# Kernel optimization log

Hardware: AMD Instinct MI355X
Metric: run time of the kernel (lower is better)

Reference implementation:

```python
import jax, jax.numpy as jnp
import numpy as np

B, S, D, H, DEG = 4, 2048, 1024, 4096, 4  # batch, seq, n_embd, hidden, chebyshev degree
LN_EPS = 1e-5


def cheb_basis(x, degree):
    """Chebyshev polynomials T_0..T_degree of x (values assumed in [-1,1]).
    x: [..., d] -> [..., d, degree+1] via the recurrence T_k = 2x T_{k-1} - T_{k-2}."""
    T = [jnp.ones_like(x), x]
    for _ in range(2, degree + 1):
        T.append(2.0 * x * T[-1] - T[-2])
    return jnp.stack(T[: degree + 1], axis=-1)


def kan_layer(x, coef, degree):
    # x: [N, in_dim], coef: [in_dim, out_dim, degree+1] -> [N, out_dim]
    basis = cheb_basis(x, degree)  # [N, in_dim, degree+1]
    return jnp.einsum('nik,iok->no', basis, coef)


def setup_inputs() -> dict:
    key = jax.random.key(0)
    k1, k2, k3 = jax.random.split(key, 3)
    x = jax.random.normal(k1, (B, S, D), dtype=jnp.float32)
    # Chebyshev-KAN coefficient init ~ N(0, 1/(in_dim*(degree+1)))
    coef_fc = jax.random.normal(k2, (D, H, DEG + 1), dtype=jnp.float32) / np.sqrt(D * (DEG + 1))
    coef_proj = jax.random.normal(k3, (H, D, DEG + 1), dtype=jnp.float32) / np.sqrt(H * (DEG + 1))
    gamma = jnp.ones((H,), dtype=jnp.float32)
    beta = jnp.zeros((H,), dtype=jnp.float32)
    return {"x": x, "coef_fc": coef_fc, "coef_proj": coef_proj, "gamma": gamma, "beta": beta}


def reference(x, coef_fc, coef_proj, gamma, beta):
    b, s, d = x.shape
    xf = jnp.tanh(x.reshape(-1, d))                 # squash into Chebyshev domain [-1,1]
    h = kan_layer(xf, coef_fc, DEG)                 # [N, H]
    mu = jnp.mean(h, axis=-1, keepdims=True)
    var = jnp.mean(jnp.square(h - mu), axis=-1, keepdims=True)
    h = (h - mu) * jax.lax.rsqrt(var + LN_EPS) * gamma + beta
    h = jnp.tanh(h)
    out = kan_layer(h, coef_proj, DEG)              # [N, D]
    return out.reshape(b, s, d)                     # dropout is identity at eval
```

## Files before the change

kernel.cpp:

```cpp
#include <hip/hip_runtime.h>
#include <hip/hip_bf16.h>
#include <cstdint>
#include <cstddef>

typedef __bf16 bf16;
typedef __attribute__((ext_vector_type(4))) __bf16 bf16x4;
typedef __attribute__((ext_vector_type(8))) __bf16 bf16x8;
typedef __attribute__((ext_vector_type(4))) float f32x4;

#define NR 8192
#define DIM_D 1024
#define DIM_H 4096


__device__ __forceinline__ void gload_lds16(const void* g, void* l) {
  __builtin_amdgcn_global_load_lds(
      (const __attribute__((address_space(1))) void*)g,
      (__attribute__((address_space(3))) void*)l, 16, 0, 0);
}

#define BAR()  __builtin_amdgcn_s_barrier()
#define WLG0() asm volatile("s_waitcnt lgkmcnt(0)" ::: "memory")
#define WVM0() asm volatile("s_waitcnt vmcnt(0)" ::: "memory")
#define WVM4() asm volatile("s_waitcnt vmcnt(4)" ::: "memory")
#define WVM6() asm volatile("s_waitcnt vmcnt(6)" ::: "memory")
#define WVM8() asm volatile("s_waitcnt vmcnt(8)" ::: "memory")
#define PRIO1() __builtin_amdgcn_s_setprio(1)
#define PRIO0() __builtin_amdgcn_s_setprio(0)


template <int IN, int OUT>
__global__ __launch_bounds__(256) void k_prep_t(const float* __restrict__ coef,
                                                bf16* __restrict__ Bp,
                                                float* __restrict__ bpart) {
  constexpr int KT = (IN / 32) * 2;
  const int tid   = threadIdx.x;
  const int o     = blockIdx.x * 256 + tid;
  const int nb    = blockIdx.x;
  const int chunk = blockIdx.y;
  const int i0    = chunk * 32;

  float bacc = 0.f;
#pragma unroll
  for (int q = 0; q < 4; ++q) {
    bf16x8 w1, w2, w3, w4;
#pragma unroll
    for (int j = 0; j < 8; ++j) {
      const float* s = coef + ((size_t)(i0 + q * 8 + j) * OUT + o) * 5;
      bacc += s[0];
      w1[j] = (bf16)s[1]; w2[j] = (bf16)s[2]; w3[j] = (bf16)s[3]; w4[j] = (bf16)s[4];
    }
    bf16* base = Bp + ((size_t)nb * KT + chunk * 2) * 16384 + (size_t)tid * 8;
    *(bf16x8*)(base + (0 * 4 + q) * 2048)         = w1;
    *(bf16x8*)(base + (1 * 4 + q) * 2048)         = w2;
    *(bf16x8*)(base + 16384 + (0 * 4 + q) * 2048) = w3;
    *(bf16x8*)(base + 16384 + (1 * 4 + q) * 2048) = w4;
  }
  bpart[(size_t)chunk * OUT + o] = bacc;
}

__global__ __launch_bounds__(256) void k_bias_red(const float* __restrict__ bpart,
                                                  float* __restrict__ bias,
                                                  const int OUT, const int NP) {
  const int o = blockIdx.x * 256 + threadIdx.x;
  float s = 0.f;
  for (int p = 0; p < NP; ++p) s += bpart[(size_t)p * OUT + o];
  bias[o] = s;
}

__global__ __launch_bounds__(256) void k_tanh_cheb_t(const float* __restrict__ x,
                                                     bf16* __restrict__ Ap) {
  const int mb    = blockIdx.x;
  const int chunk = blockIdx.y;
  const int r     = threadIdx.x;

  const float* src = x + (size_t)(mb * 256 + r) * DIM_D + chunk * 32;
  float a[32];
#pragma unroll
  for (int u = 0; u < 8; ++u) {
    const float4 v = *(const float4*)(src + u * 4);
    a[u * 4 + 0] = tanhf(v.x);
    a[u * 4 + 1] = tanhf(v.y);
    a[u * 4 + 2] = tanhf(v.z);
    a[u * 4 + 3] = tanhf(v.w);
  }
  bf16* base = Ap + ((size_t)mb * 64 + chunk * 2) * 16384 + (size_t)r * 8;
#pragma unroll
  for (int q = 0; q < 4; ++q) {
    bf16x8 w1, w2, w3, w4;
#pragma unroll
    for (int j = 0; j < 8; ++j) {
      const float t = a[q * 8 + j], t2 = t * t;
      w1[j] = (bf16)t;
      w2[j] = (bf16)(2.f * t2 - 1.f);
      w3[j] = (bf16)(t * (4.f * t2 - 3.f));
      w4[j] = (bf16)(8.f * t2 * (t2 - 1.f) + 1.f);
    }
    *(bf16x8*)(base + (0 * 4 + q) * 2048)         = w1;
    *(bf16x8*)(base + (1 * 4 + q) * 2048)         = w2;
    *(bf16x8*)(base + 16384 + (0 * 4 + q) * 2048) = w3;
    *(bf16x8*)(base + 16384 + (1 * 4 + q) * 2048) = w4;
  }
}

__global__ __launch_bounds__(256) void k_ln_tanh(const float* __restrict__ h,
                                                 const float* __restrict__ gamma,
                                                 const float* __restrict__ beta,
                                                 bf16* __restrict__ th) {
  const int n = blockIdx.x;
  const int t = threadIdx.x;
  const float* row = h + (size_t)n * DIM_H;

  float4 v[4];
  float s1 = 0.f, s2 = 0.f;
#pragma unroll
  for (int j = 0; j < 4; ++j) {
    v[j] = *(const float4*)(row + t * 16 + j * 4);
    s1 += v[j].x + v[j].y + v[j].z + v[j].w;
    s2 += v[j].x * v[j].x + v[j].y * v[j].y + v[j].z * v[j].z + v[j].w * v[j].w;
  }
#pragma unroll
  for (int off = 32; off >= 1; off >>= 1) {
    s1 += __shfl_xor(s1, off);
    s2 += __shfl_xor(s2, off);
  }
  __shared__ float red[8];
  if ((t & 63) == 0) { red[(t >> 6) * 2] = s1; red[(t >> 6) * 2 + 1] = s2; }
  __syncthreads();
  const float S1 = red[0] + red[2] + red[4] + red[6];
  const float S2 = red[1] + red[3] + red[5] + red[7];
  const float mu   = S1 * (1.f / DIM_H);
  const float var  = S2 * (1.f / DIM_H) - mu * mu;
  const float rstd = rsqrtf(var + 1e-5f);

  float tmp[16];
#pragma unroll
  for (int j = 0; j < 4; ++j) {
    const float4 g = *(const float4*)(gamma + t * 16 + j * 4);
    const float4 b = *(const float4*)(beta  + t * 16 + j * 4);
    tmp[j * 4 + 0] = tanhf((v[j].x - mu) * rstd * g.x + b.x);
    tmp[j * 4 + 1] = tanhf((v[j].y - mu) * rstd * g.y + b.y);
    tmp[j * 4 + 2] = tanhf((v[j].z - mu) * rstd * g.z + b.z);
    tmp[j * 4 + 3] = tanhf((v[j].w - mu) * rstd * g.w + b.w);
  }
  bf16x8 w0, w1;
#pragma unroll
  for (int j = 0; j < 8; ++j) { w0[j] = (bf16)tmp[j]; w1[j] = (bf16)tmp[8 + j]; }
  bf16* o = th + (size_t)n * DIM_H + t * 16;
  *(bf16x8*)o       = w0;
  *(bf16x8*)(o + 8) = w1;
}

template <int IND, int NZ, int GX, typename CT>
__global__ __launch_bounds__(512, 2) void k_gemm8x(const bf16* __restrict__ Ap,
                                                   const bf16* __restrict__ Bp,
                                                   CT* __restrict__ C,
                                                   const float* __restrict__ bias,
                                                   const int NN) {
  constexpr int NCH = IND / 32 / NZ;
  constexpr int KTt = (IND / 32) * 2;
  constexpr int TOT = GX * 32 * NZ;
  constexpr int CPX = TOT / 8;

  __shared__ bf16 Ash[2][16384];
  __shared__ bf16 Bsh[2][16384];

  const int tid  = threadIdx.x;
  const int lane = tid & 63;
  const int wid  = tid >> 6;
  const int wm   = wid >> 2;
  const int wn   = wid & 3;
  const int fr   = lane & 15;
  const int kq   = lane >> 4;

  int lin = blockIdx.x + GX * (blockIdx.y + 32 * blockIdx.z);
  lin = (lin & 7) * CPX + (lin >> 3);
  const int bx = lin % GX;
  const int by = (lin / GX) % 32;
  const int bz = lin / (GX * 32);

  const int m0  = by * 256;
  const int n0  = bx * 256;
  const int zc0 = bz * NCH;

  f32x4 acc[8][4];
#pragma unroll
  for (int m = 0; m < 8; ++m)
#pragma unroll
    for (int n = 0; n < 4; ++n) acc[m][n] = (f32x4){0.f, 0.f, 0.f, 0.f};

  const size_t bt0 = (size_t)bx * KTt + (size_t)zc0 * 2;
  const size_t at0 = (size_t)by * KTt + (size_t)zc0 * 2;

  auto stB = [&](int d, int kh, int ktl) {
    const bf16* s = Bp + (bt0 + (size_t)ktl) * 16384 + kh * 8192 + tid * 8;
    bf16* l = &Bsh[d][kh * 8192 + tid * 8];
    gload_lds16(s, l);
    gload_lds16(s + 4096, l + 4096);
  };
  auto stA = [&](int d, int kh, int ktl) {
    const bf16* s = Ap + (at0 + (size_t)ktl) * 16384 + kh * 8192 + tid * 8;
    bf16* l = &Ash[d][kh * 8192 + tid * 8];
    gload_lds16(s, l);
    gload_lds16(s + 4096, l + 4096);
  };

  bf16x8 afr[4], bfr[4];
  auto rdB = [&](int d, int kh) {
#pragma unroll
    for (int n = 0; n < 4; ++n)
      bfr[n] = *(const bf16x8*)&Bsh[d][(kh * 4 + kq) * 2048 + (wn * 64 + n * 16 + fr) * 8];
  };
  auto rdA = [&](int d, int kh, int mh) {
#pragma unroll
    for (int m = 0; m < 4; ++m)
      afr[m] = *(const bf16x8*)&Ash[d][(kh * 4 + kq) * 2048 + (wm * 128 + mh * 64 + m * 16 + fr) * 8];
  };
  auto mma = [&](int mh) {
#pragma unroll
    for (int m = 0; m < 4; ++m)
#pragma unroll
      for (int n = 0; n < 4; ++n)
        acc[mh * 4 + m][n] =
            __builtin_amdgcn_mfma_f32_16x16x32_bf16(afr[m], bfr[n], acc[mh * 4 + m][n], 0, 0, 0);
  };

  stA(0, 0, 0); stA(0, 1, 0); stB(0, 0, 0); stB(0, 1, 0);
  stA(1, 0, 1); stA(1, 1, 1); stB(1, 0, 1); stB(1, 1, 1);
  WVM8();
  BAR();

#pragma unroll 1
  for (int g = 0; g < NCH; ++g) {
    const bool st = (g + 1 < NCH);
    rdB(0, 0); rdA(0, 0, 0);
    if (g > 0) stA(1, 1, 2 * g + 1);
    BAR(); WLG0();
    PRIO1(); mma(0); PRIO0();
    BAR();
    rdA(0, 0, 1);
    if (st) stB(0, 0, 2 * g + 2);
    BAR(); WLG0();
    PRIO1(); mma(1); PRIO0();
    BAR();
    rdB(0, 1); rdA(0, 1, 0);
    if (st) stA(0, 0, 2 * g + 2);
    BAR(); WLG0();
    PRIO1(); mma(0); PRIO0();
    BAR();
    rdA(0, 1, 1);
    if (st) { stB(0, 1, 2 * g + 2); WVM6(); } else { WVM0(); }
    BAR(); WLG0();
    PRIO1(); mma(1); PRIO0();
    BAR();
    rdB(1, 0); rdA(1, 0, 0);
    if (st) stA(0, 1, 2 * g + 2);
    BAR(); WLG0();
    PRIO1(); mma(0); PRIO0();
    BAR();
    rdA(1, 0, 1);
    if (st) stB(1, 0, 2 * g + 3);
    BAR(); WLG0();
    PRIO1(); mma(1); PRIO0();
    BAR();
    rdB(1, 1); rdA(1, 1, 0);
    if (st) stA(1, 0, 2 * g + 3);
    BAR(); WLG0();
    PRIO1(); mma(0); PRIO0();
    BAR();
    rdA(1, 1, 1);
    if (st) { stB(1, 1, 2 * g + 3); WVM6(); }
    BAR(); WLG0();
    PRIO1(); mma(1); PRIO0();
    BAR();
  }

  float bv[4] = {0.f, 0.f, 0.f, 0.f};
  const int c0 = n0 + wn * 64 + fr;
  if (bias) {
#pragma unroll
    for (int n = 0; n < 4; ++n) bv[n] = bias[c0 + n * 16];
  }
  CT* Cz = C + (size_t)bz * NR * NN;
  const int r0 = m0 + wm * 128 + kq * 4;
#pragma unroll
  for (int mi = 0; mi < 8; ++mi)
#pragma unroll
    for (int j = 0; j < 4; ++j) {
      CT* p = Cz + (size_t)(r0 + mi * 16 + j) * NN + c0;
#pragma unroll
      for (int n = 0; n < 4; ++n)
        p[n * 16] = (CT)(acc[mi][n][j] + bv[n]);
    }
}

template <int IND, int NZ, int GX>
__global__ __launch_bounds__(512, 2) void k_gemm8(const bf16* __restrict__ X,
                                                  const bf16* __restrict__ Bp,
                                                  float* __restrict__ C,
                                                  const float* __restrict__ bias,
                                                  const int NN) {
  constexpr int NCH = IND / 32 / NZ;
  constexpr int KTt = (IND / 32) * 2;
  constexpr int TOT = GX * 32 * NZ;
  constexpr int CPX = TOT / 8;

  __shared__ bf16 Ash[2][16384];
  __shared__ bf16 Bsh[2][16384];

  const int tid  = threadIdx.x;
  const int lane = tid & 63;
  const int wid  = tid >> 6;
  const int wm   = wid >> 2;
  const int wn   = wid & 3;
  const int fr   = lane & 15;
  const int kq   = lane >> 4;

  int lin = blockIdx.x + GX * (blockIdx.y + 32 * blockIdx.z);
  lin = (lin & 7) * CPX + (lin >> 3);
  const int bx = lin % GX;
  const int by = (lin / GX) % 32;
  const int bz = lin / (GX * 32);

  const int m0  = by * 256;
  const int n0  = bx * 256;
  const int zc0 = bz * NCH;

  const int rA = tid & 255;
  const int qp = (tid >> 8) * 2;

  f32x4 acc[8][4];
#pragma unroll
  for (int m = 0; m < 8; ++m)
#pragma unroll
    for (int n = 0; n < 4; ++n) acc[m][n] = (f32x4){0.f, 0.f, 0.f, 0.f};

  const bf16* xp = X + (size_t)(m0 + rA) * IND + (size_t)zc0 * 32 + qp * 8;
  const size_t bt0 = (size_t)bx * KTt + (size_t)zc0 * 2;

  bf16x8 xn0, xn1;
  float  xf[16];
  bf16x8 afr[4], bfr[4];

  auto stB = [&](int d, int kh, int ktl) {
    const bf16* s = Bp + (bt0 + (size_t)ktl) * 16384 + kh * 8192 + tid * 8;
    bf16* l = &Bsh[d][kh * 8192 + tid * 8];
    gload_lds16(s, l);
    gload_lds16(s + 4096, l + 4096);
  };
  auto ldx = [&](int c) {
    const bf16* s = xp + (size_t)c * 32;
    xn0 = *(const bf16x8*)s;
    xn1 = *(const bf16x8*)(s + 8);
  };
  auto cvtxf = [&]() {
#pragma unroll
    for (int j = 0; j < 8; ++j) { xf[j] = (float)xn0[j]; xf[8 + j] = (float)xn1[j]; }
  };
  auto wA = [&](int d, int dh, bf16x8 w0, bf16x8 w1) {
    *(bf16x8*)&Ash[d][(dh * 4 + qp) * 2048 + rA * 8]     = w0;
    *(bf16x8*)&Ash[d][(dh * 4 + qp + 1) * 2048 + rA * 8] = w1;
  };
  auto chebw = [&](int deg, bf16x8& w0, bf16x8& w1) {
#pragma unroll
    for (int j = 0; j < 8; ++j) {
      const float a = xf[j], b = xf[8 + j];
      const float a2 = a * a, b2 = b * b;
      float ra, rb;
      if (deg == 2)      { ra = 2.f * a2 - 1.f;            rb = 2.f * b2 - 1.f; }
      else if (deg == 3) { ra = a * (4.f * a2 - 3.f);      rb = b * (4.f * b2 - 3.f); }
      else               { ra = 8.f * a2 * (a2 - 1.f) + 1.f; rb = 8.f * b2 * (b2 - 1.f) + 1.f; }
      w0[j] = (bf16)ra; w1[j] = (bf16)rb;
    }
  };
  auto rdB = [&](int d, int kh) {
#pragma unroll
    for (int n = 0; n < 4; ++n)
      bfr[n] = *(const bf16x8*)&Bsh[d][(kh * 4 + kq) * 2048 + (wn * 64 + n * 16 + fr) * 8];
  };
  auto rdA = [&](int d, int kh, int mh) {
#pragma unroll
    for (int m = 0; m < 4; ++m)
      afr[m] = *(const bf16x8*)&Ash[d][(kh * 4 + kq) * 2048 + (wm * 128 + mh * 64 + m * 16 + fr) * 8];
  };
  auto mma = [&](int mh) {
#pragma unroll
    for (int m = 0; m < 4; ++m)
#pragma unroll
      for (int n = 0; n < 4; ++n)
        acc[mh * 4 + m][n] =
            __builtin_amdgcn_mfma_f32_16x16x32_bf16(afr[m], bfr[n], acc[mh * 4 + m][n], 0, 0, 0);
  };

  ldx(0);
  stB(0, 0, 0); stB(0, 1, 0);
  stB(1, 0, 1); stB(1, 1, 1);
  cvtxf();
  wA(0, 0, xn0, xn1);
  { bf16x8 w0, w1; chebw(2, w0, w1); wA(0, 1, w0, w1); }
  { bf16x8 w0, w1; chebw(3, w0, w1); wA(1, 0, w0, w1); }
  { bf16x8 w0, w1; chebw(4, w0, w1); wA(1, 1, w0, w1); }
  WVM0(); WLG0();
  BAR();

#pragma unroll 1
  for (int g = 0; g < NCH; ++g) {
    const bool st = (g + 1 < NCH);
    rdB(0, 0); rdA(0, 0, 0);
    if (g > 0) { bf16x8 w0, w1; chebw(4, w0, w1); wA(1, 1, w0, w1); }
    if (st) ldx(g + 1);
    BAR(); WLG0();
    PRIO1(); mma(0); PRIO0();
    BAR();
    rdA(0, 0, 1);
    if (st) stB(0, 0, 2 * (g + 1));
    BAR(); WLG0();
    PRIO1(); mma(1); PRIO0();
    BAR();
    rdB(0, 1); rdA(0, 1, 0);
    BAR(); WLG0();
    PRIO1(); mma(0); PRIO0();
    BAR();
    rdA(0, 1, 1);
    if (st) { stB(0, 1, 2 * (g + 1)); WVM6(); } else { WVM0(); }
    BAR(); WLG0();
    PRIO1(); mma(1); PRIO0();
    BAR();
    rdB(1, 0); rdA(1, 0, 0);
    if (st) { cvtxf(); wA(0, 0, xn0, xn1); }
    BAR(); WLG0();
    PRIO1(); mma(0); PRIO0();
    BAR();
    rdA(1, 0, 1);
    if (st) { bf16x8 w0, w1; chebw(2, w0, w1); wA(0, 1, w0, w1); }
    BAR(); WLG0();
    PRIO1(); mma(1); PRIO0();
    BAR();
    rdB(1, 1); rdA(1, 1, 0);
    if (st) { bf16x8 w0, w1; chebw(3, w0, w1); wA(1, 0, w0, w1); stB(1, 0, 2 * (g + 1) + 1); }
    BAR(); WLG0();
    PRIO1(); mma(0); PRIO0();
    BAR();
    rdA(1, 1, 1);
    if (st) { stB(1, 1, 2 * (g + 1) + 1); WVM4(); }
    BAR(); WLG0();
    PRIO1(); mma(1); PRIO0();
    BAR();
  }

  float bv[4] = {0.f, 0.f, 0.f, 0.f};
  const int c0 = n0 + wn * 64 + fr;
  if (bias) {
#pragma unroll
    for (int n = 0; n < 4; ++n) bv[n] = bias[c0 + n * 16];
  }
  float* Cz = C + (size_t)bz * NR * NN;
  const int r0 = m0 + wm * 128 + kq * 4;
#pragma unroll
  for (int mi = 0; mi < 8; ++mi)
#pragma unroll
    for (int j = 0; j < 4; ++j) {
      float* p = Cz + (size_t)(r0 + mi * 16 + j) * NN + c0;
#pragma unroll
      for (int n = 0; n < 4; ++n)
        p[n * 16] = acc[mi][n][j] + bv[n];
    }
}

__global__ __launch_bounds__(256) void k_reduce2(const float* __restrict__ p0,
                                                 const float* __restrict__ p1,
                                                 const float* __restrict__ bias,
                                                 float* __restrict__ out) {
  const size_t base = (size_t)blockIdx.x * 1024 + threadIdx.x * 4;
  const float4 a = *(const float4*)(p0 + base);
  const float4 b = *(const float4*)(p1 + base);
  const float4 c = *(const float4*)(bias + threadIdx.x * 4);
  float4 r;
  r.x = a.x + b.x + c.x;
  r.y = a.y + b.y + c.y;
  r.z = a.z + b.z + c.z;
  r.w = a.w + b.w + c.w;
  *(float4*)(out + base) = r;
}


extern "C" void kernel_launch(void* const* d_in, const int* in_sizes, int n_in,
                              void* d_out, int out_size, void* d_ws, size_t ws_size,
                              hipStream_t stream) {
  const float* x         = (const float*)d_in[0];
  const float* coef_fc   = (const float*)d_in[1];
  const float* coef_proj = (const float*)d_in[2];
  const float* gamma     = (const float*)d_in[3];
  const float* beta      = (const float*)d_in[4];
  float* out = (float*)d_out;

  const size_t SZ_B  = (size_t)DIM_H * 4 * DIM_D * 2;
  const size_t SZ_A1 = (size_t)NR * DIM_D * 4 * 2;
  const size_t SZ_HF = (size_t)NR * DIM_H * 4;

  char* w = (char*)d_ws;
  bf16*  B2p   = (bf16*)w;   w += SZ_B;
  float* bias1 = (float*)w;  w += DIM_H * 4;
  float* bias2 = (float*)w;  w += DIM_D * 4;
  float* h     = (float*)w;  w += SZ_HF;
  bf16*  A1p   = (bf16*)w;   w += SZ_A1;
  bf16*  B1p   = (bf16*)w;   w += SZ_B;
  float* bpart1 = (float*)w; w += (size_t)32 * DIM_H * 4;
  float* bpart2 = (float*)w; w += (size_t)128 * DIM_D * 4;

  float* part = h;
  bf16*  th   = A1p;

  k_prep_t<DIM_D, DIM_H><<<dim3(DIM_H / 256, DIM_D / 32), 256, 0, stream>>>(coef_fc, B1p, bpart1);
  k_prep_t<DIM_H, DIM_D><<<dim3(DIM_D / 256, DIM_H / 32), 256, 0, stream>>>(coef_proj, B2p, bpart2);
  k_bias_red<<<DIM_H / 256, 256, 0, stream>>>(bpart1, bias1, DIM_H, DIM_D / 32);
  k_bias_red<<<DIM_D / 256, 256, 0, stream>>>(bpart2, bias2, DIM_D, DIM_H / 32);

  k_tanh_cheb_t<<<dim3(NR / 256, DIM_D / 32), 256, 0, stream>>>(x, A1p);

  k_gemm8x<DIM_D, 1, 16, float><<<dim3(DIM_H / 256, NR / 256, 1), 512, 0, stream>>>(
      A1p, B1p, h, bias1, DIM_H);

  k_ln_tanh<<<NR, 256, 0, stream>>>(h, gamma, beta, th);

  k_gemm8<DIM_H, 2, 4><<<dim3(DIM_D / 256, NR / 256, 2), 512, 0, stream>>>(
      th, B2p, part, nullptr, DIM_D);
  k_reduce2<<<NR, 256, 0, stream>>>(part, part + (size_t)NR * DIM_D, bias2, out);
}
```

Baseline: 687.5 us.

## Store hidden in bf16, split LayerNorm, pre-expand Chebyshev basis for second GEMM

The first GEMM now writes the hidden activations in bf16 instead of fp32. LayerNorm is split into a per-row stats kernel and a fused LN+tanh+Chebyshev expansion kernel that writes the packed A operand. The second GEMM then reuses the generic packed-A kernel with 4-way split-K, runs in two row halves to bound workspace, and writes bf16 partials that a 4-way reduce sums with the bias. The explicit lgkmcnt(0) waits after each barrier are also removed. The aim is less fp32 traffic and a simpler GEMM inner loop. The cost is writing and re-reading a large expanded basis buffer, plus precision loss from bf16 hidden values and bf16 partial sums.

```diff
diff --git a/kernel.cpp b/kernel.cpp
--- a/kernel.cpp
+++ b/kernel.cpp
@@ -20,9 +20,7 @@
 }
 
 #define BAR()  __builtin_amdgcn_s_barrier()
-#define WLG0() asm volatile("s_waitcnt lgkmcnt(0)" ::: "memory")
 #define WVM0() asm volatile("s_waitcnt vmcnt(0)" ::: "memory")
-#define WVM4() asm volatile("s_waitcnt vmcnt(4)" ::: "memory")
 #define WVM6() asm volatile("s_waitcnt vmcnt(6)" ::: "memory")
 #define WVM8() asm volatile("s_waitcnt vmcnt(8)" ::: "memory")
 #define PRIO1() __builtin_amdgcn_s_setprio(1)
@@ -103,21 +101,22 @@
   }
 }
 
-__global__ __launch_bounds__(256) void k_ln_tanh(const float* __restrict__ h,
-                                                 const float* __restrict__ gamma,
-                                                 const float* __restrict__ beta,
-                                                 bf16* __restrict__ th) {
+__global__ __launch_bounds__(256) void k_ln_stats(const bf16* __restrict__ h,
+                                                  float2* __restrict__ stats) {
   const int n = blockIdx.x;
   const int t = threadIdx.x;
-  const float* row = h + (size_t)n * DIM_H;
-
-  float4 v[4];
+  const bf16* row = h + (size_t)n * DIM_H;
+
   float s1 = 0.f, s2 = 0.f;
-#pragma unroll
-  for (int j = 0; j < 4; ++j) {
-    v[j] = *(const float4*)(row + t * 16 + j * 4);
-    s1 += v[j].x + v[j].y + v[j].z + v[j].w;
-    s2 += v[j].x * v[j].x + v[j].y * v[j].y + v[j].z * v[j].z + v[j].w * v[j].w;
+  {
+    const bf16x8 a = *(const bf16x8*)(row + t * 16);
+    const bf16x8 b = *(const bf16x8*)(row + t * 16 + 8);
+#pragma unroll
+    for (int j = 0; j < 8; ++j) {
+      const float va = (float)a[j], vb = (float)b[j];
+      s1 += va + vb;
+      s2 += va * va + vb * vb;
+    }
   }
 #pragma unroll
   for (int off = 32; off >= 1; off >>= 1) {
@@ -127,39 +126,66 @@
   __shared__ float red[8];
   if ((t & 63) == 0) { red[(t >> 6) * 2] = s1; red[(t >> 6) * 2 + 1] = s2; }
   __syncthreads();
-  const float S1 = red[0] + red[2] + red[4] + red[6];
-  const float S2 = red[1] + red[3] + red[5] + red[7];
-  const float mu   = S1 * (1.f / DIM_H);
-  const float var  = S2 * (1.f / DIM_H) - mu * mu;
-  const float rstd = rsqrtf(var + 1e-5f);
-
-  float tmp[16];
-#pragma unroll
-  for (int j = 0; j < 4; ++j) {
-    const float4 g = *(const float4*)(gamma + t * 16 + j * 4);
-    const float4 b = *(const float4*)(beta  + t * 16 + j * 4);
-    tmp[j * 4 + 0] = tanhf((v[j].x - mu) * rstd * g.x + b.x);
-    tmp[j * 4 + 1] = tanhf((v[j].y - mu) * rstd * g.y + b.y);
-    tmp[j * 4 + 2] = tanhf((v[j].z - mu) * rstd * g.z + b.z);
-    tmp[j * 4 + 3] = tanhf((v[j].w - mu) * rstd * g.w + b.w);
-  }
-  bf16x8 w0, w1;
-#pragma unroll
-  for (int j = 0; j < 8; ++j) { w0[j] = (bf16)tmp[j]; w1[j] = (bf16)tmp[8 + j]; }
-  bf16* o = th + (size_t)n * DIM_H + t * 16;
-  *(bf16x8*)o       = w0;
-  *(bf16x8*)(o + 8) = w1;
-}
-
-template <int IND, int NZ, int GX, typename CT>
+  if (t == 0) {
+    const float S1 = red[0] + red[2] + red[4] + red[6];
+    const float S2 = red[1] + red[3] + red[5] + red[7];
+    const float mu  = S1 * (1.f / DIM_H);
+    const float var = S2 * (1.f / DIM_H) - mu * mu;
+    stats[n] = make_float2(mu, rsqrtf(var + 1e-5f));
+  }
+}
+
+__global__ __launch_bounds__(256) void k_lntanh_cheb_t(const bf16* __restrict__ h,
+                                                       const float2* __restrict__ stats,
+                                                       const float* __restrict__ gamma,
+                                                       const float* __restrict__ beta,
+                                                       bf16* __restrict__ Ap) {
+  const int mb    = blockIdx.x;
+  const int chunk = blockIdx.y;
+  const int r     = threadIdx.x;
+  const int row   = mb * 256 + r;
+
+  const float2 st = stats[row];
+  const bf16* src = h + (size_t)row * DIM_H + chunk * 32;
+
+  float f[32];
+#pragma unroll
+  for (int q = 0; q < 4; ++q) {
+    const bf16x8 v = *(const bf16x8*)(src + q * 8);
+#pragma unroll
+    for (int j = 0; j < 8; ++j) {
+      const int c = chunk * 32 + q * 8 + j;
+      f[q * 8 + j] = tanhf(((float)v[j] - st.x) * st.y * gamma[c] + beta[c]);
+    }
+  }
+  bf16* base = Ap + ((size_t)mb * 256 + chunk * 2) * 16384 + (size_t)r * 8;
+#pragma unroll
+  for (int q = 0; q < 4; ++q) {
+    bf16x8 w1, w2, w3, w4;
+#pragma unroll
+    for (int j = 0; j < 8; ++j) {
+      const float t = f[q * 8 + j], t2 = t * t;
+      w1[j] = (bf16)t;
+      w2[j] = (bf16)(2.f * t2 - 1.f);
+      w3[j] = (bf16)(t * (4.f * t2 - 3.f));
+      w4[j] = (bf16)(8.f * t2 * (t2 - 1.f) + 1.f);
+    }
+    *(bf16x8*)(base + (0 * 4 + q) * 2048)         = w1;
+    *(bf16x8*)(base + (1 * 4 + q) * 2048)         = w2;
+    *(bf16x8*)(base + 16384 + (0 * 4 + q) * 2048) = w3;
+    *(bf16x8*)(base + 16384 + (1 * 4 + q) * 2048) = w4;
+  }
+}
+
+template <int IND, int NZ, int GX, int GY, typename CT>
 __global__ __launch_bounds__(512, 2) void k_gemm8x(const bf16* __restrict__ Ap,
                                                    const bf16* __restrict__ Bp,
                                                    CT* __restrict__ C,
                                                    const float* __restrict__ bias,
-                                                   const int NN) {
+                                                   const int NN, const int MR) {
   constexpr int NCH = IND / 32 / NZ;
   constexpr int KTt = (IND / 32) * 2;
-  constexpr int TOT = GX * 32 * NZ;
+  constexpr int TOT = GX * GY * NZ;
   constexpr int CPX = TOT / 8;
 
   __shared__ bf16 Ash[2][16384];
@@ -173,11 +199,11 @@
   const int fr   = lane & 15;
   const int kq   = lane >> 4;
 
-  int lin = blockIdx.x + GX * (blockIdx.y + 32 * blockIdx.z);
+  int lin = blockIdx.x + GX * (blockIdx.y + GY * blockIdx.z);
   lin = (lin & 7) * CPX + (lin >> 3);
   const int bx = lin % GX;
-  const int by = (lin / GX) % 32;
-  const int bz = lin / (GX * 32);
+  const int by = (lin / GX) % GY;
+  const int bz = lin / (GX * GY);
 
   const int m0  = by * 256;
   const int n0  = bx * 256;
@@ -235,42 +261,42 @@
     const bool st = (g + 1 < NCH);
     rdB(0, 0); rdA(0, 0, 0);
     if (g > 0) stA(1, 1, 2 * g + 1);
-    BAR(); WLG0();
+    BAR();
     PRIO1(); mma(0); PRIO0();
     BAR();
     rdA(0, 0, 1);
     if (st) stB(0, 0, 2 * g + 2);
-    BAR(); WLG0();
+    BAR();
     PRIO1(); mma(1); PRIO0();
     BAR();
     rdB(0, 1); rdA(0, 1, 0);
     if (st) stA(0, 0, 2 * g + 2);
-    BAR(); WLG0();
+    BAR();
     PRIO1(); mma(0); PRIO0();
     BAR();
     rdA(0, 1, 1);
     if (st) { stB(0, 1, 2 * g + 2); WVM6(); } else { WVM0(); }
-    BAR(); WLG0();
+    BAR();
     PRIO1(); mma(1); PRIO0();
     BAR();
     rdB(1, 0); rdA(1, 0, 0);
     if (st) stA(0, 1, 2 * g + 2);
-    BAR(); WLG0();
+    BAR();
     PRIO1(); mma(0); PRIO0();
     BAR();
     rdA(1, 0, 1);
     if (st) stB(1, 0, 2 * g + 3);
-    BAR(); WLG0();
+    BAR();
     PRIO1(); mma(1); PRIO0();
     BAR();
     rdB(1, 1); rdA(1, 1, 0);
     if (st) stA(1, 0, 2 * g + 3);
-    BAR(); WLG0();
+    BAR();
     PRIO1(); mma(0); PRIO0();
     BAR();
     rdA(1, 1, 1);
     if (st) { stB(1, 1, 2 * g + 3); WVM6(); }
-    BAR(); WLG0();
+    BAR();
     PRIO1(); mma(1); PRIO0();
     BAR();
   }
@@ -281,7 +307,7 @@
 #pragma unroll
     for (int n = 0; n < 4; ++n) bv[n] = bias[c0 + n * 16];
   }
-  CT* Cz = C + (size_t)bz * NR * NN;
+  CT* Cz = C + (size_t)bz * MR * NN;
   const int r0 = m0 + wm * 128 + kq * 4;
 #pragma unroll
   for (int mi = 0; mi < 8; ++mi)
@@ -294,192 +320,18 @@
     }
 }
 
-template <int IND, int NZ, int GX>
-__global__ __launch_bounds__(512, 2) void k_gemm8(const bf16* __restrict__ X,
-                                                  const bf16* __restrict__ Bp,
-                                                  float* __restrict__ C,
-                                                  const float* __restrict__ bias,
-                                                  const int NN) {
-  constexpr int NCH = IND / 32 / NZ;
-  constexpr int KTt = (IND / 32) * 2;
-  constexpr int TOT = GX * 32 * NZ;
-  constexpr int CPX = TOT / 8;
-
-  __shared__ bf16 Ash[2][16384];
-  __shared__ bf16 Bsh[2][16384];
-
-  const int tid  = threadIdx.x;
-  const int lane = tid & 63;
-  const int wid  = tid >> 6;
-  const int wm   = wid >> 2;
-  const int wn   = wid & 3;
-  const int fr   = lane & 15;
-  const int kq   = lane >> 4;
-
-  int lin = blockIdx.x + GX * (blockIdx.y + 32 * blockIdx.z);
-  lin = (lin & 7) * CPX + (lin >> 3);
-  const int bx = lin % GX;
-  const int by = (lin / GX) % 32;
-  const int bz = lin / (GX * 32);
-
-  const int m0  = by * 256;
-  const int n0  = bx * 256;
-  const int zc0 = bz * NCH;
-
-  const int rA = tid & 255;
-  const int qp = (tid >> 8) * 2;
-
-  f32x4 acc[8][4];
-#pragma unroll
-  for (int m = 0; m < 8; ++m)
-#pragma unroll
-    for (int n = 0; n < 4; ++n) acc[m][n] = (f32x4){0.f, 0.f, 0.f, 0.f};
-
-  const bf16* xp = X + (size_t)(m0 + rA) * IND + (size_t)zc0 * 32 + qp * 8;
-  const size_t bt0 = (size_t)bx * KTt + (size_t)zc0 * 2;
-
-  bf16x8 xn0, xn1;
-  float  xf[16];
-  bf16x8 afr[4], bfr[4];
-
-  auto stB = [&](int d, int kh, int ktl) {
-    const bf16* s = Bp + (bt0 + (size_t)ktl) * 16384 + kh * 8192 + tid * 8;
-    bf16* l = &Bsh[d][kh * 8192 + tid * 8];
-    gload_lds16(s, l);
-    gload_lds16(s + 4096, l + 4096);
-  };
-  auto ldx = [&](int c) {
-    const bf16* s = xp + (size_t)c * 32;
-    xn0 = *(const bf16x8*)s;
-    xn1 = *(const bf16x8*)(s + 8);
-  };
-  auto cvtxf = [&]() {
-#pragma unroll
-    for (int j = 0; j < 8; ++j) { xf[j] = (float)xn0[j]; xf[8 + j] = (float)xn1[j]; }
-  };
-  auto wA = [&](int d, int dh, bf16x8 w0, bf16x8 w1) {
-    *(bf16x8*)&Ash[d][(dh * 4 + qp) * 2048 + rA * 8]     = w0;
-    *(bf16x8*)&Ash[d][(dh * 4 + qp + 1) * 2048 + rA * 8] = w1;
-  };
-  auto chebw = [&](int deg, bf16x8& w0, bf16x8& w1) {
-#pragma unroll
-    for (int j = 0; j < 8; ++j) {
-      const float a = xf[j], b = xf[8 + j];
-      const float a2 = a * a, b2 = b * b;
-      float ra, rb;
-      if (deg == 2)      { ra = 2.f * a2 - 1.f;            rb = 2.f * b2 - 1.f; }
-      else if (deg == 3) { ra = a * (4.f * a2 - 3.f);      rb = b * (4.f * b2 - 3.f); }
-      else               { ra = 8.f * a2 * (a2 - 1.f) + 1.f; rb = 8.f * b2 * (b2 - 1.f) + 1.f; }
-      w0[j] = (bf16)ra; w1[j] = (bf16)rb;
-    }
-  };
-  auto rdB = [&](int d, int kh) {
-#pragma unroll
-    for (int n = 0; n < 4; ++n)
-      bfr[n] = *(const bf16x8*)&Bsh[d][(kh * 4 + kq) * 2048 + (wn * 64 + n * 16 + fr) * 8];
-  };
-  auto rdA = [&](int d, int kh, int mh) {
-#pragma unroll
-    for (int m = 0; m < 4; ++m)
-      afr[m] = *(const bf16x8*)&Ash[d][(kh * 4 + kq) * 2048 + (wm * 128 + mh * 64 + m * 16 + fr) * 8];
-  };
-  auto mma = [&](int mh) {
-#pragma unroll
-    for (int m = 0; m < 4; ++m)
-#pragma unroll
-      for (int n = 0; n < 4; ++n)
-        acc[mh * 4 + m][n] =
-            __builtin_amdgcn_mfma_f32_16x16x32_bf16(afr[m], bfr[n], acc[mh * 4 + m][n], 0, 0, 0);
-  };
-
-  ldx(0);
-  stB(0, 0, 0); stB(0, 1, 0);
-  stB(1, 0, 1); stB(1, 1, 1);
-  cvtxf();
-  wA(0, 0, xn0, xn1);
-  { bf16x8 w0, w1; chebw(2, w0, w1); wA(0, 1, w0, w1); }
-  { bf16x8 w0, w1; chebw(3, w0, w1); wA(1, 0, w0, w1); }
-  { bf16x8 w0, w1; chebw(4, w0, w1); wA(1, 1, w0, w1); }
-  WVM0(); WLG0();
-  BAR();
-
-#pragma unroll 1
-  for (int g = 0; g < NCH; ++g) {
-    const bool st = (g + 1 < NCH);
-    rdB(0, 0); rdA(0, 0, 0);
-    if (g > 0) { bf16x8 w0, w1; chebw(4, w0, w1); wA(1, 1, w0, w1); }
-    if (st) ldx(g + 1);
-    BAR(); WLG0();
-    PRIO1(); mma(0); PRIO0();
-    BAR();
-    rdA(0, 0, 1);
-    if (st) stB(0, 0, 2 * (g + 1));
-    BAR(); WLG0();
-    PRIO1(); mma(1); PRIO0();
-    BAR();
-    rdB(0, 1); rdA(0, 1, 0);
-    BAR(); WLG0();
-    PRIO1(); mma(0); PRIO0();
-    BAR();
-    rdA(0, 1, 1);
-    if (st) { stB(0, 1, 2 * (g + 1)); WVM6(); } else { WVM0(); }
-    BAR(); WLG0();
-    PRIO1(); mma(1); PRIO0();
-    BAR();
-    rdB(1, 0); rdA(1, 0, 0);
-    if (st) { cvtxf(); wA(0, 0, xn0, xn1); }
-    BAR(); WLG0();
-    PRIO1(); mma(0); PRIO0();
-    BAR();
-    rdA(1, 0, 1);
-    if (st) { bf16x8 w0, w1; chebw(2, w0, w1); wA(0, 1, w0, w1); }
-    BAR(); WLG0();
-    PRIO1(); mma(1); PRIO0();
-    BAR();
-    rdB(1, 1); rdA(1, 1, 0);
-    if (st) { bf16x8 w0, w1; chebw(3, w0, w1); wA(1, 0, w0, w1); stB(1, 0, 2 * (g + 1) + 1); }
-    BAR(); WLG0();
-    PRIO1(); mma(0); PRIO0();
-    BAR();
-    rdA(1, 1, 1);
-    if (st) { stB(1, 1, 2 * (g + 1) + 1); WVM4(); }
-    BAR(); WLG0();
-    PRIO1(); mma(1); PRIO0();
-    BAR();
-  }
-
-  float bv[4] = {0.f, 0.f, 0.f, 0.f};
-  const int c0 = n0 + wn * 64 + fr;
-  if (bias) {
-#pragma unroll
-    for (int n = 0; n < 4; ++n) bv[n] = bias[c0 + n * 16];
-  }
-  float* Cz = C + (size_t)bz * NR * NN;
-  const int r0 = m0 + wm * 128 + kq * 4;
-#pragma unroll
-  for (int mi = 0; mi < 8; ++mi)
-#pragma unroll
-    for (int j = 0; j < 4; ++j) {
-      float* p = Cz + (size_t)(r0 + mi * 16 + j) * NN + c0;
-#pragma unroll
-      for (int n = 0; n < 4; ++n)
-        p[n * 16] = acc[mi][n][j] + bv[n];
-    }
-}
-
-__global__ __launch_bounds__(256) void k_reduce2(const float* __restrict__ p0,
-                                                 const float* __restrict__ p1,
+__global__ __launch_bounds__(256) void k_reduce4(const bf16* __restrict__ part,
                                                  const float* __restrict__ bias,
                                                  float* __restrict__ out) {
-  const size_t base = (size_t)blockIdx.x * 1024 + threadIdx.x * 4;
-  const float4 a = *(const float4*)(p0 + base);
-  const float4 b = *(const float4*)(p1 + base);
-  const float4 c = *(const float4*)(bias + threadIdx.x * 4);
-  float4 r;
-  r.x = a.x + b.x + c.x;
-  r.y = a.y + b.y + c.y;
-  r.z = a.z + b.z + c.z;
-  r.w = a.w + b.w + c.w;
+  const int row = blockIdx.x;
+  const int c   = threadIdx.x * 4;
+  const size_t base = (size_t)row * 1024 + c;
+  float4 r = *(const float4*)(bias + c);
+#pragma unroll
+  for (int z = 0; z < 4; ++z) {
+    const bf16x4 p = *(const bf16x4*)(part + (size_t)z * 4096 * 1024 + base);
+    r.x += (float)p[0]; r.y += (float)p[1]; r.z += (float)p[2]; r.w += (float)p[3];
+  }
   *(float4*)(out + base) = r;
 }
 
@@ -494,36 +346,45 @@
   const float* beta      = (const float*)d_in[4];
   float* out = (float*)d_out;
 
-  const size_t SZ_B  = (size_t)DIM_H * 4 * DIM_D * 2;
-  const size_t SZ_A1 = (size_t)NR * DIM_D * 4 * 2;
-  const size_t SZ_HF = (size_t)NR * DIM_H * 4;
+  const size_t SZ_B   = (size_t)DIM_H * 4 * DIM_D * 2;
+  const size_t SZ_HB  = (size_t)NR * DIM_H * 2;
+  const size_t SZ_A2H = (size_t)(NR / 2) * DIM_H * 4 * 2;
+  const size_t SZ_A1  = (size_t)NR * DIM_D * 4 * 2;
+  const size_t SZ_PT  = (size_t)4 * (NR / 2) * DIM_D * 2;
 
   char* w = (char*)d_ws;
-  bf16*  B2p   = (bf16*)w;   w += SZ_B;
-  float* bias1 = (float*)w;  w += DIM_H * 4;
-  float* bias2 = (float*)w;  w += DIM_D * 4;
-  float* h     = (float*)w;  w += SZ_HF;
-  bf16*  A1p   = (bf16*)w;   w += SZ_A1;
-  bf16*  B1p   = (bf16*)w;   w += SZ_B;
-  float* bpart1 = (float*)w; w += (size_t)32 * DIM_H * 4;
-  float* bpart2 = (float*)w; w += (size_t)128 * DIM_D * 4;
-
-  float* part = h;
-  bf16*  th   = A1p;
+  bf16*   B2p   = (bf16*)w;    w += SZ_B;
+  float*  bias1 = (float*)w;   w += DIM_H * 4;
+  float*  bias2 = (float*)w;   w += DIM_D * 4;
+  float2* stats = (float2*)w;  w += (size_t)NR * 8;
+  bf16*   h     = (bf16*)w;    w += SZ_HB;
+  char*   R3    = w;           w += SZ_A2H;
+  bf16*   part  = (bf16*)w;    w += SZ_PT;
+
+  bf16*  A1p    = (bf16*)R3;
+  bf16*  B1p    = (bf16*)(R3 + SZ_A1);
+  float* bpart1 = (float*)(R3 + SZ_A1 + SZ_B);
+  float* bpart2 = (float*)(R3 + SZ_A1 + SZ_B + (size_t)32 * DIM_H * 4);
+  bf16*  A2p    = (bf16*)R3;
 
   k_prep_t<DIM_D, DIM_H><<<dim3(DIM_H / 256, DIM_D / 32), 256, 0, stream>>>(coef_fc, B1p, bpart1);
   k_prep_t<DIM_H, DIM_D><<<dim3(DIM_D / 256, DIM_H / 32), 256, 0, stream>>>(coef_proj, B2p, bpart2);
   k_bias_red<<<DIM_H / 256, 256, 0, stream>>>(bpart1, bias1, DIM_H, DIM_D / 32);
   k_bias_red<<<DIM_D / 256, 256, 0, stream>>>(bpart2, bias2, DIM_D, DIM_H / 32);
-
   k_tanh_cheb_t<<<dim3(NR / 256, DIM_D / 32), 256, 0, stream>>>(x, A1p);
 
-  k_gemm8x<DIM_D, 1, 16, float><<<dim3(DIM_H / 256, NR / 256, 1), 512, 0, stream>>>(
-      A1p, B1p, h, bias1, DIM_H);
-
-  k_ln_tanh<<<NR, 256, 0, stream>>>(h, gamma, beta, th);
-
-  k_gemm8<DIM_H, 2, 4><<<dim3(DIM_D / 256, NR / 256, 2), 512, 0, stream>>>(
-      th, B2p, part, nullptr, DIM_D);
-  k_reduce2<<<NR, 256, 0, stream>>>(part, part + (size_t)NR * DIM_D, bias2, out);
-}
+  k_gemm8x<DIM_D, 1, 16, 32, bf16><<<dim3(16, 32, 1), 512, 0, stream>>>(
+      A1p, B1p, h, bias1, DIM_H, NR);
+
+  k_ln_stats<<<NR, 256, 0, stream>>>(h, stats);
+
+  for (int half = 0; half < 2; ++half) {
+    const bf16*   hh = h + (size_t)half * (NR / 2) * DIM_H;
+    const float2* sh = stats + (size_t)half * (NR / 2);
+    k_lntanh_cheb_t<<<dim3(16, DIM_H / 32), 256, 0, stream>>>(hh, sh, gamma, beta, A2p);
+    k_gemm8x<DIM_H, 4, 4, 16, bf16><<<dim3(4, 16, 4), 512, 0, stream>>>(
+        A2p, B2p, part, nullptr, DIM_D, NR / 2);
+    k_reduce4<<<NR / 2, 256, 0, stream>>>(part, bias2,
+                                          out + (size_t)half * (NR / 2) * DIM_D);
+  }
+}
```

Result: faster. 664.7 us (-3.3%).
